# Kernel optimization log

Measured on AMD Instinct MI355X. Metric: run time of the kernel, lower is better.

Reference implementation:

```python
import jax, jax.numpy as jnp
import numpy as np
import math


def setup_inputs() -> dict:
    key = jax.random.key(0)
    ks = jax.random.split(key, 10)
    B, N, C, heads = 16, 1024, 256, 8
    nW = 4
    ANGLE_BINS = 5
    inner = C  # dim_head*heads == dim
    return {
        "x": jax.random.normal(ks[0], (B, N, C), jnp.float32),
        "mask": jax.random.normal(ks[1], (nW, N, N), jnp.float32),
        "affine_matrix": jax.random.normal(ks[2], (B, 2, 3), jnp.float32),
        "Wq": jax.random.normal(ks[3], (C, inner), jnp.float32) * (C ** -0.5),
        "bq": jnp.zeros((inner,), jnp.float32),
        "Wkv": jax.random.normal(ks[4], (C, 2 * inner), jnp.float32) * (C ** -0.5),
        "bkv": jnp.zeros((2 * inner,), jnp.float32),
        "Wp": jax.random.normal(ks[5], (C, C), jnp.float32) * (C ** -0.5),
        "bp": jnp.zeros((C,), jnp.float32),
        "angle_table": jnp.ones((ANGLE_BINS, heads), jnp.float32),
        "H": 32,
        "W": 32,
    }


def reference(x, mask, affine_matrix, Wq, bq, Wkv, bkv, Wp, bp, angle_table, H, W):
    B, N, C = x.shape
    heads = angle_table.shape[1]
    hd = C // heads
    scale = hd ** -0.5

    # qkv projections (torch Linear -> x @ W + b with W stored as (in, out))
    q = (x @ Wq + bq).reshape(B, N, heads, hd).transpose(0, 2, 1, 3)      # (B,h,N,d)
    kv = (x @ Wkv + bkv).reshape(B, N, 2, heads, hd).transpose(2, 0, 3, 1, 4)
    k, v = kv[0], kv[1]                                                    # (B,h,N,d)

    attn = jnp.einsum('bhqd,bhkd->bhqk', q * scale, k)                     # (B,h,N,N)

    # angle bias: per-query multiplicative bias in (1,2)
    grid_y, grid_x = jnp.meshgrid(jnp.arange(H), jnp.arange(W), indexing='ij')
    coords = jnp.stack([grid_x.reshape(-1), grid_y.reshape(-1)], -1).astype(jnp.float32)  # (N,2)
    center = jnp.array([W / 2.0, H / 2.0], jnp.float32)
    ego = jnp.einsum('bij,j->bi', affine_matrix[:, :2, :2], center) + affine_matrix[:, :2, 2]  # (B,2)
    rel = coords[None, :, :] - ego[:, None, :]                             # (B,N,2)
    ang = jnp.arctan2(rel[..., 1], rel[..., 0])
    bins = (((ang + math.pi) / (2.0 * math.pi)) * (angle_table.shape[0] - 1)).astype(jnp.int32)
    bias = 1.0 + jax.nn.sigmoid(angle_table[bins])                         # (B,N,h)
    attn = attn * bias.transpose(0, 2, 1)[..., None]                       # broadcast over keys

    # additive window mask then softmax
    nW = mask.shape[0]
    attn = attn.reshape(B // nW, nW, heads, N, N) + mask[None, :, None]
    attn = jax.nn.softmax(attn.reshape(B, heads, N, N), axis=-1)

    out = jnp.einsum('bhqk,bhkd->bhqd', attn, v).transpose(0, 2, 1, 3).reshape(B, N, C)
    return out @ Wp + bp
```

## Files before the change

kernel.cpp:

```cpp
#include <hip/hip_runtime.h>
#include <hip/hip_bf16.h>
#include <math.h>

#define BB 16
#define NTOK 1024
#define CDIM 256
#define HEADS 8
#define HD 32
#define LOG2E 1.4426950408889634f
#define PSHIFT 18.0f

typedef __attribute__((ext_vector_type(8))) _Float16 half8;
typedef __attribute__((ext_vector_type(8))) unsigned short u16x8;
typedef __attribute__((ext_vector_type(4))) unsigned int u32x4;
typedef __attribute__((ext_vector_type(2))) unsigned int u32x2;
typedef __attribute__((ext_vector_type(4))) float f32x4;

__device__ __forceinline__ unsigned short f2h(float f) {
  _Float16 h = (_Float16)f;
  return __builtin_bit_cast(unsigned short, h);
}
__device__ __forceinline__ half8 ldh8(const unsigned short* p) {
  return *reinterpret_cast<const half8*>(p);
}
__device__ __forceinline__ void gl_lds16(const unsigned short* g,
                                         unsigned short* l) {
  __builtin_amdgcn_global_load_lds(
      (const __attribute__((address_space(1))) unsigned int*)g,
      (__attribute__((address_space(3))) unsigned int*)l, 16, 0, 0);
}

__global__ __launch_bounds__(256) void cvt_x(const float* __restrict__ X,
                                             unsigned short* __restrict__ x16) {
  size_t base = ((size_t)blockIdx.x * 256 + threadIdx.x) * 8;
  float4 a = *(const float4*)(X + base);
  float4 b = *(const float4*)(X + base + 4);
  u16x8 o = {f2h(a.x), f2h(a.y), f2h(a.z), f2h(a.w),
             f2h(b.x), f2h(b.y), f2h(b.z), f2h(b.w)};
  *(u16x8*)(x16 + base) = o;
}

__global__ __launch_bounds__(256) void cvt_w(
    const float* __restrict__ Wq, const float* __restrict__ Wkv,
    const float* __restrict__ Wp, unsigned short* __restrict__ wt16,
    unsigned short* __restrict__ wp16) {
  int idx = blockIdx.x * 256 + threadIdx.x;
  float val; size_t dst; bool isp = false;
  if (idx < 65536) {
    int k = idx >> 8, n = idx & 255;
    val = Wq[idx]; dst = (size_t)n * 256 + k;
  } else if (idx < 196608) {
    int i2 = idx - 65536;
    int k = i2 >> 9, n2 = i2 & 511;
    val = Wkv[i2]; dst = (size_t)(256 + n2) * 256 + k;
  } else {
    int i3 = idx - 196608;
    int k = i3 >> 8, n = i3 & 255;
    val = Wp[i3]; dst = (size_t)n * 256 + k; isp = true;
  }
  unsigned short h = f2h(val);
  if (isp) wp16[dst] = h; else wt16[dst] = h;
}

__global__ __launch_bounds__(256) void bias_kernel(
    const float* __restrict__ affine, const float* __restrict__ atab,
    float* __restrict__ bias) {
  int idx = blockIdx.x * 256 + threadIdx.x;
  if (idx >= BB * NTOK) return;
  int b = idx >> 10, n = idx & (NTOK - 1);
  float cx = (float)(n & 31);
  float cy = (float)(n >> 5);
  const float* A = affine + b * 6;
  float egx = fmaf(A[0], 16.f, fmaf(A[1], 16.f, A[2]));
  float egy = fmaf(A[3], 16.f, fmaf(A[4], 16.f, A[5]));
  float ang = atan2f(cy - egy, cx - egx);
  float t = (ang + 3.14159265358979323846f) *
            (1.f / (2.f * 3.14159265358979323846f)) * 4.f;
  int bin = (int)t;
  bin = bin < 0 ? 0 : (bin > 4 ? 4 : bin);
  for (int h = 0; h < HEADS; ++h) {
    float a = atab[bin * HEADS + h];
    float s = 1.f / (1.f + __expf(-a));
    bias[((size_t)b * HEADS + h) * NTOK + n] = 1.f + s;
  }
}

__global__ __launch_bounds__(256) void mask_prepF(const float* __restrict__ m,
                                                  float* __restrict__ mF) {
  int idx = blockIdx.x * 256 + threadIdx.x;
  int b4 = idx >> 18;
  int rem = idx & 262143;
  int q = rem >> 8;
  int k = (rem & 255) * 4;
  float4 v = *(const float4*)(m + ((size_t)b4 * NTOK + q) * NTOK + k);
  float4 o = {fmaf(v.x, LOG2E, -PSHIFT), fmaf(v.y, LOG2E, -PSHIFT),
              fmaf(v.z, LOG2E, -PSHIFT), fmaf(v.w, LOG2E, -PSHIFT)};
  int kt = k >> 6, f = (k >> 4) & 3, ins = k & 15;
  size_t dst = ((size_t)((b4 * 16 + kt) * 4 + f)) * 16384 + q * 16 + ins;
  *(float4*)(mF + dst) = o;
}

__device__ __forceinline__ int off16(int row, int g) {
  int R = row >> 1;
  int p = (((row & 1) << 2) | g) ^ (R & 7);
  return R * 64 + p * 8;
}

__global__ __launch_bounds__(512, 4) void gemm_qkv16(
    const unsigned short* __restrict__ x16, const unsigned short* __restrict__ wt16,
    const float* __restrict__ bq, const float* __restrict__ bkv,
    const float* __restrict__ bias, unsigned short* __restrict__ q16,
    unsigned short* __restrict__ k16, unsigned short* __restrict__ vt16) {
  __shared__ __align__(16) unsigned short SM[24576];
  unsigned short* Xs = SM;
  unsigned short* Ws = SM + 12288;
  int tid = threadIdx.x;
  int w = tid >> 6, l = tid & 63;
  int row16 = l & 15, grp = l >> 4;
  int bid = blockIdx.x;
  int xcd = bid & 7, local = bid >> 3;
  int jb = local % 6, mb = xcd * 16 + local / 6;
  int j0 = jb * 128, m0 = mb * 128;
  int wm = w >> 1, wn = w & 1;

  auto stg = [&](int nb, int kt) {
    int k0s = (kt & 7) * 32;
    int R = w * 8 + (l >> 3);
    int q = (l & 7) ^ (R & 7);
    int row = 2 * R + (q >> 2);
    int ce = (q & 3) * 8;
    gl_lds16(x16 + (size_t)(m0 + row) * 256 + k0s + ce, Xs + nb * 4096 + w * 512);
    gl_lds16(wt16 + (size_t)(j0 + row) * 256 + k0s + ce, Ws + nb * 4096 + w * 512);
  };

  stg(0, 0);
  stg(1, 1);

  f32x4 acc[2][4];
#pragma unroll
  for (int i = 0; i < 2; ++i)
#pragma unroll
    for (int c = 0; c < 4; ++c) acc[i][c] = (f32x4){0.f, 0.f, 0.f, 0.f};

  for (int kt = 0; kt < 8; ++kt) {
    int cur = kt % 3;
    asm volatile("s_waitcnt vmcnt(2)" ::: "memory");
    __builtin_amdgcn_s_barrier();
    stg((kt + 2) % 3, kt + 2);
    half8 a0 = ldh8(Xs + cur * 4096 + off16(wm * 32 + row16, grp));
    half8 a1 = ldh8(Xs + cur * 4096 + off16(wm * 32 + 16 + row16, grp));
#pragma unroll
    for (int c = 0; c < 4; ++c) {
      half8 bh = ldh8(Ws + cur * 4096 + off16(wn * 64 + c * 16 + row16, grp));
      acc[0][c] = __builtin_amdgcn_mfma_f32_16x16x32_f16(a0, bh, acc[0][c], 0, 0, 0);
      acc[1][c] = __builtin_amdgcn_mfma_f32_16x16x32_f16(a1, bh, acc[1][c], 0, 0, 0);
    }
  }
  asm volatile("s_waitcnt vmcnt(0)" ::: "memory");
  __syncthreads();

  const float scaleq = 0.17677669529663687f * LOG2E;
  int half_mine = wm >> 1;
  for (int half = 0; half < 2; ++half) {
    if (half_mine == half) {
#pragma unroll
      for (int i = 0; i < 2; ++i) {
#pragma unroll
        for (int c = 0; c < 4; ++c) {
          int col = wn * 64 + c * 16 + row16;
          int jg = j0 + col;
#pragma unroll
          for (int r = 0; r < 4; ++r) {
            int rowl = (wm & 1) * 32 + i * 16 + grp * 4 + r;
            int m = m0 + half * 64 + rowl;
            int b = m >> 10, n = m & (NTOK - 1);
            float val = acc[i][c][r];
            unsigned short o;
            if (jb < 2)
              o = f2h((val + bq[jg]) * scaleq *
                      bias[((size_t)b * HEADS + (jg >> 5)) * NTOK + n]);
            else
              o = f2h(val + bkv[jg - CDIM]);
            SM[rowl * 136 + col] = o;
          }
        }
      }
    }
    __syncthreads();
    if (jb < 4) {
#pragma unroll
      for (int it = 0; it < 2; ++it) {
        int lin = it * 512 + tid;
        int rowb = lin >> 4, oct = lin & 15;
        u16x8 v = *(const u16x8*)&SM[rowb * 136 + oct * 8];
        int m = m0 + half * 64 + rowb;
        int b = m >> 10, n = m & (NTOK - 1);
        int jg = j0 + oct * 8;
        unsigned short* dst; int h, d;
        if (jb < 2) { h = jg >> 5; d = jg & 31; dst = q16; }
        else { int c2 = jg - CDIM; h = c2 >> 5; d = c2 & 31; dst = k16; }
        *(u16x8*)(dst + (((size_t)b * HEADS + h) * NTOK + n) * HD + d) = v;
      }
    } else {
#pragma unroll
      for (int it = 0; it < 2; ++it) {
        int lin = it * 512 + tid;
        int noct = lin >> 7, jl = lin & 127;
        u16x8 v;
#pragma unroll
        for (int e = 0; e < 8; ++e) v[e] = SM[(noct * 8 + e) * 136 + jl];
        int c3 = j0 + jl - 2 * CDIM;
        int h = c3 >> 5, d = c3 & 31;
        int n0 = m0 + half * 64 + noct * 8;
        int b = n0 >> 10, nn = n0 & (NTOK - 1);
        *(u16x8*)(vt16 + (((size_t)b * HEADS + h) * HD + d) * NTOK + nn) = v;
      }
    }
    __syncthreads();
  }
}

__global__ __launch_bounds__(512, 8) void attn16(
    const unsigned short* __restrict__ q16, const unsigned short* __restrict__ k16,
    const unsigned short* __restrict__ vt16, const float* __restrict__ maskF,
    unsigned short* __restrict__ ao16) {
  __shared__ __align__(16) unsigned short KT[3][2048];
  __shared__ __align__(16) unsigned short VT[3][2048];
  __shared__ __align__(16) unsigned Pp[8][16][20];

  int tid = threadIdx.x;
  int w = tid >> 6, l = tid & 63;
  int row16 = l & 15, grp = l >> 4;
  int bid = blockIdx.x;
  int swz = (bid & 7) * 128 + (bid >> 3);
  int qt = swz & 7, h = (swz >> 3) & 7, b = swz >> 6;
  int q0 = qt * 128;
  int bh = b * HEADS + h;

  size_t qidx = (((size_t)bh * NTOK) + q0 + w * 16 + row16) * HD + grp * 8;
  half8 bq16 = ldh8(q16 + qidx);

  const float* mFb = maskF + (size_t)(b & 3) * 64 * 16384 +
                     (q0 + w * 16 + row16) * 16 + grp * 4;

  f32x4 accd[2];
  accd[0] = (f32x4){0.f, 0.f, 0.f, 0.f};
  accd[1] = (f32x4){0.f, 0.f, 0.f, 0.f};
  float lsum = 0.f;

  auto stage = [&](int nbuf, int kt2) {
    int k0n = (kt2 & 15) * 64;
    if (w < 4) {
      int R = w * 8 + (l >> 3);
      int q = (l & 7) ^ (R & 7);
      int row = 2 * R + (q >> 2);
      int col = (q & 3) * 8;
      gl_lds16(k16 + (((size_t)bh * NTOK) + k0n + row) * HD + col,
               &KT[nbuf][w * 512]);
    } else {
      int sub = w - 4;
      int dl = sub * 8 + (l >> 3);
      int gk = (((l & 7) * 16) ^ ((dl & 7) << 4)) >> 1;
      gl_lds16(vt16 + ((size_t)bh * HD + dl) * NTOK + k0n + gk,
               &VT[nbuf][sub * 512]);
    }
  };

  stage(0, 0);
  stage(1, 1);

  for (int kt = 0; kt < 16; ++kt) {
    int cur = kt % 3;
    asm volatile("s_waitcnt vmcnt(1)" ::: "memory");
    __builtin_amdgcn_s_barrier();

    f32x4 mC[4];
#pragma unroll
    for (int f = 0; f < 4; ++f)
      mC[f] = *(const f32x4*)(mFb + (size_t)(kt * 4 + f) * 16384);
    __builtin_amdgcn_sched_barrier(0);
    stage((kt + 2) % 3, kt + 2);

#pragma unroll
    for (int hf = 0; hf < 2; ++hf) {
      f32x4 s[2];
#pragma unroll
      for (int fp = 0; fp < 2; ++fp) {
        int f = hf * 2 + fp;
        int kl = f * 16 + row16;
        half8 kf = ldh8(&KT[cur][off16(kl, grp)]);
        s[fp] = __builtin_amdgcn_mfma_f32_16x16x32_f16(kf, bq16, mC[f], 0, 0, 0);
      }
#pragma unroll
      for (int fp = 0; fp < 2; ++fp) {
        float p0 = __builtin_amdgcn_exp2f(s[fp][0]);
        float p1 = __builtin_amdgcn_exp2f(s[fp][1]);
        float p2 = __builtin_amdgcn_exp2f(s[fp][2]);
        float p3 = __builtin_amdgcn_exp2f(s[fp][3]);
        lsum += (p0 + p1) + (p2 + p3);
        unsigned pk01 =
            __builtin_bit_cast(unsigned, __builtin_amdgcn_cvt_pkrtz(p0, p1));
        unsigned pk23 =
            __builtin_bit_cast(unsigned, __builtin_amdgcn_cvt_pkrtz(p2, p3));
        *(u32x2*)&Pp[w][row16][fp * 8 + grp * 2] = (u32x2){pk01, pk23};
      }
      half8 pa =
          __builtin_bit_cast(half8, *(const u32x4*)&Pp[w][row16][grp * 4]);
#pragma unroll
      for (int df = 0; df < 2; ++df) {
        int dl = df * 16 + row16;
        int cb = (hf * 64 + grp * 16) ^ ((dl & 7) << 4);
        half8 v = ldh8(&VT[cur][dl * 64 + (cb >> 1)]);
        accd[df] = __builtin_amdgcn_mfma_f32_16x16x32_f16(pa, v, accd[df], 0, 0, 0);
      }
    }
  }
  asm volatile("s_waitcnt vmcnt(0)" ::: "memory");

  lsum += __shfl_xor(lsum, 16);
  lsum += __shfl_xor(lsum, 32);
#pragma unroll
  for (int r = 0; r < 4; ++r) {
    float lr = __shfl(lsum, grp * 4 + r, 16);
    float inv = 1.f / lr;
    int qrow = q0 + w * 16 + grp * 4 + r;
    size_t obase = ((size_t)b * NTOK + qrow) * CDIM + h * HD;
    ao16[obase + row16] = f2h(accd[0][r] * inv);
    ao16[obase + 16 + row16] = f2h(accd[1][r] * inv);
  }
}

__global__ __launch_bounds__(512, 4) void gemm_out16(
    const unsigned short* __restrict__ a16, const unsigned short* __restrict__ wp16,
    const float* __restrict__ bp, float* __restrict__ out) {
  __shared__ __align__(16) unsigned short SM[24576];
  unsigned short* Xs = SM;
  unsigned short* Ws = SM + 12288;
  int tid = threadIdx.x;
  int w = tid >> 6, l = tid & 63;
  int row16 = l & 15, grp = l >> 4;
  int bid = blockIdx.x;
  int xcd = bid & 7, local = bid >> 3;
  int jb = local & 1, mb = xcd * 16 + (local >> 1);
  int j0 = jb * 128, m0 = mb * 128;
  int wm = w >> 1, wn = w & 1;

  auto stg = [&](int nb, int kt) {
    int k0s = (kt & 7) * 32;
    int R = w * 8 + (l >> 3);
    int q = (l & 7) ^ (R & 7);
    int row = 2 * R + (q >> 2);
    int ce = (q & 3) * 8;
    gl_lds16(a16 + (size_t)(m0 + row) * 256 + k0s + ce, Xs + nb * 4096 + w * 512);
    gl_lds16(wp16 + (size_t)(j0 + row) * 256 + k0s + ce, Ws + nb * 4096 + w * 512);
  };

  stg(0, 0);
  stg(1, 1);

  f32x4 acc[2][4];
#pragma unroll
  for (int i = 0; i < 2; ++i)
#pragma unroll
    for (int c = 0; c < 4; ++c) acc[i][c] = (f32x4){0.f, 0.f, 0.f, 0.f};

  for (int kt = 0; kt < 8; ++kt) {
    int cur = kt % 3;
    asm volatile("s_waitcnt vmcnt(2)" ::: "memory");
    __builtin_amdgcn_s_barrier();
    stg((kt + 2) % 3, kt + 2);
    half8 a0 = ldh8(Xs + cur * 4096 + off16(wm * 32 + row16, grp));
    half8 a1 = ldh8(Xs + cur * 4096 + off16(wm * 32 + 16 + row16, grp));
#pragma unroll
    for (int c = 0; c < 4; ++c) {
      half8 bh = ldh8(Ws + cur * 4096 + off16(wn * 64 + c * 16 + row16, grp));
      acc[0][c] = __builtin_amdgcn_mfma_f32_16x16x32_f16(a0, bh, acc[0][c], 0, 0, 0);
      acc[1][c] = __builtin_amdgcn_mfma_f32_16x16x32_f16(a1, bh, acc[1][c], 0, 0, 0);
    }
  }
  asm volatile("s_waitcnt vmcnt(0)" ::: "memory");

#pragma unroll
  for (int i = 0; i < 2; ++i) {
    int ng = m0 + wm * 32 + i * 16 + grp * 4;
#pragma unroll
    for (int c = 0; c < 4; ++c) {
      int jg = j0 + wn * 64 + c * 16 + row16;
      float bias = bp[jg];
#pragma unroll
      for (int r = 0; r < 4; ++r) {
        out[(size_t)(ng + r) * CDIM + jg] = acc[i][c][r] + bias;
      }
    }
  }
}

extern "C" void kernel_launch(void* const* d_in, const int* in_sizes, int n_in,
                              void* d_out, int out_size, void* d_ws,
                              size_t ws_size, hipStream_t stream) {
  const float* x = (const float*)d_in[0];
  const float* mask = (const float*)d_in[1];
  const float* affine = (const float*)d_in[2];
  const float* Wq = (const float*)d_in[3];
  const float* bq = (const float*)d_in[4];
  const float* Wkv = (const float*)d_in[5];
  const float* bkv = (const float*)d_in[6];
  const float* Wp = (const float*)d_in[7];
  const float* bp = (const float*)d_in[8];
  const float* atab = (const float*)d_in[9];
  float* out = (float*)d_out;

  const size_t bhnd = (size_t)BB * HEADS * NTOK * HD;
  unsigned short* q16 = (unsigned short*)d_ws;
  unsigned short* k16 = q16 + bhnd;
  unsigned short* vt16 = k16 + bhnd;
  unsigned short* x16 = vt16 + bhnd;
  unsigned short* wt16 = x16 + bhnd;
  unsigned short* wp16 = wt16 + 768 * 256;
  float* bias = (float*)(wp16 + 256 * 256);
  float* maskF = bias + (size_t)BB * HEADS * NTOK;

  cvt_x<<<2048, 256, 0, stream>>>(x, x16);
  cvt_w<<<1024, 256, 0, stream>>>(Wq, Wkv, Wp, wt16, wp16);
  bias_kernel<<<64, 256, 0, stream>>>(affine, atab, bias);
  mask_prepF<<<4096, 256, 0, stream>>>(mask, maskF);
  gemm_qkv16<<<768, 512, 0, stream>>>(x16, wt16, bq, bkv, bias, q16, k16, vt16);
  attn16<<<1024, 512, 0, stream>>>(q16, k16, vt16, maskF, x16);
  gemm_out16<<<256, 512, 0, stream>>>(x16, wp16, bp, out);
}
```

Measured before the change: 100.3 us.

## Interleave key rows so softmax probabilities feed PV MFMA directly from registers

```diff
diff --git a/kernel.cpp b/kernel.cpp
--- a/kernel.cpp
+++ b/kernel.cpp
@@ -13,7 +13,6 @@
 typedef __attribute__((ext_vector_type(8))) _Float16 half8;
 typedef __attribute__((ext_vector_type(8))) unsigned short u16x8;
 typedef __attribute__((ext_vector_type(4))) unsigned int u32x4;
-typedef __attribute__((ext_vector_type(2))) unsigned int u32x2;
 typedef __attribute__((ext_vector_type(4))) float f32x4;
 
 __device__ __forceinline__ unsigned short f2h(float f) {
@@ -95,9 +94,12 @@
   float4 v = *(const float4*)(m + ((size_t)b4 * NTOK + q) * NTOK + k);
   float4 o = {fmaf(v.x, LOG2E, -PSHIFT), fmaf(v.y, LOG2E, -PSHIFT),
               fmaf(v.z, LOG2E, -PSHIFT), fmaf(v.w, LOG2E, -PSHIFT)};
-  int kt = k >> 6, f = (k >> 4) & 3, ins = k & 15;
-  size_t dst = ((size_t)((b4 * 16 + kt) * 4 + f)) * 16384 + q * 16 + ins;
-  *(float4*)(mF + dst) = o;
+  int kt = k >> 6, hf = (k >> 5) & 1, a = (k & 31) >> 2;
+  size_t base = ((size_t)((b4 * 16 + kt) * 4 + hf * 2)) * 16384 + q * 16 + a * 2;
+  float2 e = {o.x, o.z};
+  float2 d = {o.y, o.w};
+  *(float2*)(mF + base) = e;
+  *(float2*)(mF + base + 16384) = d;
 }
 
 __device__ __forceinline__ int off16(int row, int g) {
@@ -226,7 +228,6 @@
     unsigned short* __restrict__ ao16) {
   __shared__ __align__(16) unsigned short KT[3][2048];
   __shared__ __align__(16) unsigned short VT[3][2048];
-  __shared__ __align__(16) unsigned Pp[8][16][20];
 
   int tid = threadIdx.x;
   int w = tid >> 6, l = tid & 63;
@@ -286,26 +287,25 @@
       f32x4 s[2];
 #pragma unroll
       for (int fp = 0; fp < 2; ++fp) {
-        int f = hf * 2 + fp;
-        int kl = f * 16 + row16;
+        int kl = hf * 32 + 2 * row16 + fp;
         half8 kf = ldh8(&KT[cur][off16(kl, grp)]);
-        s[fp] = __builtin_amdgcn_mfma_f32_16x16x32_f16(kf, bq16, mC[f], 0, 0, 0);
-      }
-#pragma unroll
-      for (int fp = 0; fp < 2; ++fp) {
-        float p0 = __builtin_amdgcn_exp2f(s[fp][0]);
-        float p1 = __builtin_amdgcn_exp2f(s[fp][1]);
-        float p2 = __builtin_amdgcn_exp2f(s[fp][2]);
-        float p3 = __builtin_amdgcn_exp2f(s[fp][3]);
-        lsum += (p0 + p1) + (p2 + p3);
-        unsigned pk01 =
-            __builtin_bit_cast(unsigned, __builtin_amdgcn_cvt_pkrtz(p0, p1));
-        unsigned pk23 =
-            __builtin_bit_cast(unsigned, __builtin_amdgcn_cvt_pkrtz(p2, p3));
-        *(u32x2*)&Pp[w][row16][fp * 8 + grp * 2] = (u32x2){pk01, pk23};
-      }
-      half8 pa =
-          __builtin_bit_cast(half8, *(const u32x4*)&Pp[w][row16][grp * 4]);
+        s[fp] = __builtin_amdgcn_mfma_f32_16x16x32_f16(kf, bq16,
+                                                       mC[hf * 2 + fp], 0, 0, 0);
+      }
+      f32x4 e0, e1;
+#pragma unroll
+      for (int r = 0; r < 4; ++r) {
+        e0[r] = __builtin_amdgcn_exp2f(s[0][r]);
+        e1[r] = __builtin_amdgcn_exp2f(s[1][r]);
+      }
+      lsum += ((e0[0] + e1[0]) + (e0[1] + e1[1])) +
+              ((e0[2] + e1[2]) + (e0[3] + e1[3]));
+      u32x4 pk;
+#pragma unroll
+      for (int r = 0; r < 4; ++r)
+        pk[r] = __builtin_bit_cast(unsigned,
+                                   __builtin_amdgcn_cvt_pkrtz(e0[r], e1[r]));
+      half8 pa = __builtin_bit_cast(half8, pk);
 #pragma unroll
       for (int df = 0; df < 2; ++df) {
         int dl = df * 16 + row16;
```

After: 306.9 us. 3.06x slower.
